# Performance work log

Hardware: AMD Instinct MI355X
Metric: run time of the kernel (lower is better)

## Reference

```python
import math
import jax, jax.numpy as jnp
import numpy as np


def _local_crf(F_w, Q, k):
    # F_w: [B, k*k, H, W] per-pixel filter weights; Q: [B, C, H, W]
    # out[b,c,i,j] = sum_p F_w[b,p,i,j] * Q[b,c,i+di(p)-pad, j+dj(p)-pad] (zero pad)
    B, C, H, W = Q.shape
    pad = k // 2
    Qp = jnp.pad(Q, ((0, 0), (0, 0), (pad, pad), (pad, pad)))
    out = jnp.zeros_like(Q)
    for p in range(k * k):  # small fixed loop over kernel taps, fused by XLA
        di, dj = p // k, p % k
        out = out + F_w[:, p:p + 1] * Qp[:, :, di:di + H, dj:dj + W]
    return out


def setup_inputs() -> dict:
    key = jax.random.key(0)
    k1, k2, k3 = jax.random.split(key, 3)
    B, C, H, W = 4, 150, 320, 320
    klen = 7
    input_F = jax.random.uniform(k1, (B, klen * klen, H, W), dtype=jnp.float32)
    input_logit = jax.random.normal(k2, (B, C, H, W), dtype=jnp.float32)
    # learned compatibility param, init uniform(-0.05, 0.05) as in reset_parameters
    compatibility = jax.random.uniform(k3, (C, C, 1, 1), dtype=jnp.float32,
                                       minval=-0.05, maxval=0.05)
    return {"input_F": input_F, "input_logit": input_logit,
            "compatibility": compatibility}


def reference(input_F, input_logit, compatibility):
    kernel_size = input_F.shape[1]
    k = int(round(math.sqrt(kernel_size)))
    assert k * k == kernel_size
    Q = jax.nn.softmax(input_logit, axis=1)
    out = _local_crf(input_F, Q, k)
    comp = jax.nn.sigmoid(100.0 * compatibility)  # learning_compatibility=True
    # 1x1 conv: weight [C_out, C_in, 1, 1]
    out = jnp.einsum('oi,bihw->bohw', comp[:, :, 0, 0], out)
    return input_logit - out
```

## Files before the change

kernel.cpp:

```cpp
#include <hip/hip_runtime.h>
#include <math.h>

#define BB 4
#define CC 150
#define HH 320
#define WW 320
#define HW (HH*WW)
#define KP 49

typedef unsigned int uint32;
typedef unsigned short u16;
typedef short bf16x8 __attribute__((ext_vector_type(8)));
typedef float f32x4 __attribute__((ext_vector_type(4)));
typedef uint32 u32x4 __attribute__((ext_vector_type(4)));

__device__ inline u16 f2bf(float x) {
    union { float f; uint32 u; } v; v.f = x;
    uint32 r = v.u + 0x7FFFu + ((v.u >> 16) & 1u);
    return (u16)(r >> 16);
}
__device__ inline void unpk(uint32 d, float* w) {
    union { uint32 u; float f; } a, b;
    a.u = d << 16; b.u = d & 0xFFFF0000u;
    w[0] = a.f; w[1] = b.f;
}

__global__ void k0_prep(const float* __restrict__ comp, u16* __restrict__ compA) {
    int idx = blockIdx.x * 256 + threadIdx.x;
    if (idx < 160 * 160) {
        int o = idx / 160;
        int k = idx - o * 160;
        float r = 0.f;
        if (o < CC && k < CC) {
            float v = comp[o * CC + k];
            r = 1.0f / (1.0f + __expf(-100.0f * v));
        }
        compA[idx] = f2bf(r);
    }
}

__global__ __launch_bounds__(256) void k1_softmax_mix(
    const float* __restrict__ logit, const u16* __restrict__ compA,
    u16* __restrict__ R)
{
    __shared__ __align__(16) u16 Qb[20][64][8];
    __shared__ float red[4][64];

    const int tid = threadIdx.x;
    const int p   = tid & 63;
    const int g   = tid >> 6;
    const int b   = blockIdx.y;
    const int pix0 = blockIdx.x * 64;

    const float* src = logit + (size_t)b * CC * HW + pix0 + p;

    float ev[38];
    float s = 0.f;
#pragma unroll
    for (int k = 0; k < 38; ++k) {
        int c = g + 4 * k;
        float e = 0.f;
        if (c < CC) e = __expf(src[(size_t)c * HW]);
        ev[k] = e;
        s += e;
    }
    red[g][p] = s;
    if (tid < 64) {
        *(uint32*)&Qb[18][tid][6] = 0u;
        *(u32x4*)&Qb[19][tid][0] = (u32x4){0u, 0u, 0u, 0u};
    }
    __syncthreads();
    const float inv = 1.0f / (red[0][p] + red[1][p] + red[2][p] + red[3][p]);
#pragma unroll
    for (int k = 0; k < 38; ++k) {
        int c = g + 4 * k;
        if (c < CC) Qb[c >> 3][p][c & 7] = f2bf(ev[k] * inv);
    }
    __syncthreads();

    const int n    = p & 15;
    const int quad = p >> 4;

    f32x4 acc[10];
#pragma unroll
    for (int mt = 0; mt < 10; ++mt) acc[mt] = (f32x4){0.f, 0.f, 0.f, 0.f};

#pragma unroll
    for (int ks = 0; ks < 5; ++ks) {
        bf16x8 bfrag = *(const bf16x8*)&Qb[ks * 4 + quad][g * 16 + n][0];
#pragma unroll
        for (int mt = 0; mt < 10; ++mt) {
            bf16x8 afrag = *(const bf16x8*)(compA + (mt * 16 + n) * 160
                                            + ks * 32 + quad * 8);
            acc[mt] = __builtin_amdgcn_mfma_f32_16x16x32_bf16(afrag, bfrag,
                                                              acc[mt], 0, 0, 0);
        }
    }

    u16* dst = R + (size_t)b * CC * HW + pix0 + g * 16 + n;
#pragma unroll
    for (int mt = 0; mt < 10; ++mt) {
#pragma unroll
        for (int r = 0; r < 4; ++r) {
            int o = mt * 16 + quad * 4 + r;
            if (o < CC) dst[(size_t)o * HW] = f2bf(acc[mt][r]);
        }
    }
}

#define HT 32
#define WT 64
#define OB 6
#define RROWS 38
#define RSTR 72
#define RPLANE (RROWS * RSTR)

__global__ __launch_bounds__(256) void k3_crf(
    const float* __restrict__ F, const float* __restrict__ logit,
    const u16* __restrict__ R, float* __restrict__ out)
{
    __shared__ __align__(16) u16 Rs[OB * RPLANE];

    const int tid = threadIdx.x;
    const int tx = tid & 7;
    const int ty = tid >> 3;
    const int zz = blockIdx.z;
    const int b  = zz / 25;
    const int oc = (zz - b * 25) * OB;
    const int i0 = blockIdx.y * HT;
    const int j0 = blockIdx.x * WT;
    const int i  = i0 + ty;
    const int jb = j0 + tx * 8;

    const u16*   Rb = R     + (size_t)b * CC * HW;
    const float* Fb = F     + (size_t)b * KP * HW + (size_t)i * WW + jb;
    const float* Lb = logit + (size_t)b * CC * HW;
    float*       Ob = out   + (size_t)b * CC * HW;

    for (int idx = tid; idx < OB * RROWS * 36; idx += 256) {
        int u   = idx / (RROWS * 36);
        int rem = idx - u * (RROWS * 36);
        int r   = rem / 36;
        int c2  = rem - r * 36;
        int gi  = i0 - 3 + r;
        int gj  = j0 - 4 + 2 * c2;
        uint32 v = 0u;
        if (gi >= 0 && gi < HH && gj >= 0 && gj < WW)
            v = *(const uint32*)(Rb + (size_t)(oc + u) * HW + gi * WW + gj);
        *(uint32*)&Rs[u * RPLANE + r * RSTR + 2 * c2] = v;
    }
    __syncthreads();

    float acc[OB][8];
#pragma unroll
    for (int u = 0; u < OB; ++u)
#pragma unroll
        for (int q = 0; q < 8; ++q) acc[u][q] = 0.f;

#pragma unroll
    for (int di = 0; di < 7; ++di) {
        f32x4 fa[7], fb[7];
#pragma unroll
        for (int dj = 0; dj < 7; ++dj) {
            const float* fp = Fb + (size_t)(di * 7 + dj) * HW;
            fa[dj] = *(const f32x4*)(fp);
            fb[dj] = *(const f32x4*)(fp + 4);
        }
#pragma unroll
        for (int u = 0; u < OB; ++u) {
            const uint32* wp = (const uint32*)&Rs[u * RPLANE + (ty + di) * RSTR
                                                 + tx * 8];
            u32x4 wa = *(const u32x4*)wp;
            u32x4 wb = *(const u32x4*)(wp + 4);
            float w[16];
            unpk(wa.x, w + 0);  unpk(wa.y, w + 2);
            unpk(wa.z, w + 4);  unpk(wa.w, w + 6);
            unpk(wb.x, w + 8);  unpk(wb.y, w + 10);
            unpk(wb.z, w + 12); unpk(wb.w, w + 14);
#pragma unroll
            for (int dj = 0; dj < 7; ++dj) {
                acc[u][0] = fmaf(fa[dj].x, w[1 + 0 + dj], acc[u][0]);
                acc[u][1] = fmaf(fa[dj].y, w[1 + 1 + dj], acc[u][1]);
                acc[u][2] = fmaf(fa[dj].z, w[1 + 2 + dj], acc[u][2]);
                acc[u][3] = fmaf(fa[dj].w, w[1 + 3 + dj], acc[u][3]);
                acc[u][4] = fmaf(fb[dj].x, w[5 + 0 + dj], acc[u][4]);
                acc[u][5] = fmaf(fb[dj].y, w[5 + 1 + dj], acc[u][5]);
                acc[u][6] = fmaf(fb[dj].z, w[5 + 2 + dj], acc[u][6]);
                acc[u][7] = fmaf(fb[dj].w, w[5 + 3 + dj], acc[u][7]);
            }
        }
    }

#pragma unroll
    for (int u = 0; u < OB; ++u) {
        size_t off = (size_t)(oc + u) * HW + (size_t)i * WW + jb;
        f32x4 l0 = __builtin_nontemporal_load((const f32x4*)(Lb + off));
        f32x4 l1 = __builtin_nontemporal_load((const f32x4*)(Lb + off) + 1);
        f32x4 o0, o1;
        o0.x = l0.x - acc[u][0]; o0.y = l0.y - acc[u][1];
        o0.z = l0.z - acc[u][2]; o0.w = l0.w - acc[u][3];
        o1.x = l1.x - acc[u][4]; o1.y = l1.y - acc[u][5];
        o1.z = l1.z - acc[u][6]; o1.w = l1.w - acc[u][7];
        __builtin_nontemporal_store(o0, (f32x4*)(Ob + off));
        __builtin_nontemporal_store(o1, (f32x4*)(Ob + off) + 1);
    }
}

extern "C" void kernel_launch(void* const* d_in, const int* in_sizes, int n_in,
                              void* d_out, int out_size, void* d_ws, size_t ws_size,
                              hipStream_t stream)
{
    const float* dF = (const float*)d_in[0];
    const float* dL = (const float*)d_in[1];
    const float* dC = (const float*)d_in[2];

    u16* compA = (u16*)d_ws;
    u16* R     = (u16*)((char*)d_ws + (1 << 16));
    float* o   = (float*)d_out;

    hipLaunchKernelGGL(k0_prep, dim3((160 * 160 + 255) / 256), dim3(256), 0,
                       stream, dC, compA);
    hipLaunchKernelGGL(k1_softmax_mix, dim3(HW / 64, BB), dim3(256), 0, stream,
                       dL, compA, R);
    hipLaunchKernelGGL(k3_crf, dim3(WW / WT, HH / HT, BB * 25), dim3(256), 0,
                       stream, dF, dL, R, o);
}
```

Before: 1.068 ms.

## Stage mix output through LDS for coalesced stores and remap CRF blocks per XCD

The softmax-mix kernel now assigns each thread group a contiguous channel range, so it can write packed bf16 pairs into shared memory. Its MFMA outputs are staged through LDS and written to global memory as 16-byte coalesced rows instead of scattered 2-byte stores. The CRF kernel remaps its linear block index so all channel chunks of one spatial tile land on the same XCD, which should improve L2 reuse of F. It also adds a launch-bounds occupancy hint of 4. The price is extra syncs and LDS traffic in k1, and possible register spilling in k3 under the new bound.

```diff
diff --git a/kernel.cpp b/kernel.cpp
--- a/kernel.cpp
+++ b/kernel.cpp
@@ -58,7 +58,7 @@
     float s = 0.f;
 #pragma unroll
     for (int k = 0; k < 38; ++k) {
-        int c = g + 4 * k;
+        int c = 38 * g + k;
         float e = 0.f;
         if (c < CC) e = __expf(src[(size_t)c * HW]);
         ev[k] = e;
@@ -72,9 +72,13 @@
     __syncthreads();
     const float inv = 1.0f / (red[0][p] + red[1][p] + red[2][p] + red[3][p]);
 #pragma unroll
-    for (int k = 0; k < 38; ++k) {
-        int c = g + 4 * k;
-        if (c < CC) Qb[c >> 3][p][c & 7] = f2bf(ev[k] * inv);
+    for (int k = 0; k < 38; k += 2) {
+        int c = 38 * g + k;
+        if (c < CC) {
+            uint32 w = (uint32)f2bf(ev[k] * inv)
+                     | ((uint32)f2bf(ev[k + 1] * inv) << 16);
+            *(uint32*)&Qb[c >> 3][p][c & 7] = w;
+        }
     }
     __syncthreads();
 
@@ -97,14 +101,22 @@
         }
     }
 
-    u16* dst = R + (size_t)b * CC * HW + pix0 + g * 16 + n;
+    __syncthreads();
+    u16* S = &Qb[0][0][0];
 #pragma unroll
     for (int mt = 0; mt < 10; ++mt) {
 #pragma unroll
         for (int r = 0; r < 4; ++r) {
             int o = mt * 16 + quad * 4 + r;
-            if (o < CC) dst[(size_t)o * HW] = f2bf(acc[mt][r]);
-        }
+            if (o < CC) S[o * 64 + g * 16 + n] = f2bf(acc[mt][r]);
+        }
+    }
+    __syncthreads();
+    u16* dstB = R + (size_t)b * CC * HW + pix0;
+    for (int idx = tid; idx < CC * 8; idx += 256) {
+        int o = idx >> 3, seg = idx & 7;
+        *(u32x4*)(dstB + (size_t)o * HW + seg * 8) =
+            *(const u32x4*)&S[o * 64 + seg * 8];
     }
 }
 
@@ -115,7 +127,7 @@
 #define RSTR 72
 #define RPLANE (RROWS * RSTR)
 
-__global__ __launch_bounds__(256) void k3_crf(
+__global__ __launch_bounds__(256, 4) void k3_crf(
     const float* __restrict__ F, const float* __restrict__ logit,
     const u16* __restrict__ R, float* __restrict__ out)
 {
@@ -124,11 +136,21 @@
     const int tid = threadIdx.x;
     const int tx = tid & 7;
     const int ty = tid >> 3;
-    const int zz = blockIdx.z;
-    const int b  = zz / 25;
-    const int oc = (zz - b * 25) * OB;
-    const int i0 = blockIdx.y * HT;
-    const int j0 = blockIdx.x * WT;
+
+    const uint32 lin  = blockIdx.x + 5u * blockIdx.y + 50u * blockIdx.z;
+    const uint32 xcd  = lin & 7u;
+    const uint32 sl   = lin >> 3;
+    const uint32 tl   = sl / 25u;
+    const uint32 chnk = sl - tl * 25u;
+    const uint32 tile = xcd * 25u + tl;
+    const int btx = (int)(tile % 5u);
+    const uint32 t2 = tile / 5u;
+    const int bty = (int)(t2 % 10u);
+    const int b   = (int)(t2 / 10u);
+    const int oc  = (int)chnk * OB;
+
+    const int i0 = bty * HT;
+    const int j0 = btx * WT;
     const int i  = i0 + ty;
     const int jb = j0 + tx * 8;
 
```

Measured after the change: 1.969 ms. 84.3% more time.
